# Kernel optimization log

Measured on AMD Instinct MI355X. Metric: run time of the kernel, lower is better.

Reference implementation:

```python
import jax, jax.numpy as jnp
import numpy as np

N_NODES = 50000
N_HEDGES = 10000
N_MEMB = 800000
IN_SIZE = 256
HEADS = 4
OUT_SIZE = 64


def setup_inputs() -> dict:
    key = jax.random.key(0)
    k1, k2, k3, k4, k5 = jax.random.split(key, 5)
    x = jax.random.normal(k1, (N_NODES, IN_SIZE), dtype=jnp.float32)
    # Linear weight stored as [in, out*heads] so projection is x @ W (same math as torch Linear)
    W = jax.random.normal(k2, (IN_SIZE, OUT_SIZE * HEADS), dtype=jnp.float32) * (1.0 / np.sqrt(IN_SIZE))
    att_e = jax.random.normal(k3, (1, HEADS, OUT_SIZE), dtype=jnp.float32) * 0.1
    node_idx = jax.random.randint(k4, (N_MEMB,), 0, N_NODES, dtype=jnp.int64)
    hedge_idx = jax.random.randint(k5, (N_MEMB,), 0, N_HEDGES, dtype=jnp.int64)
    return {"x": x, "W": W, "att_e": att_e, "node_idx": node_idx,
            "hedge_idx": hedge_idx, "num_hyperedges": N_HEDGES}


def reference(x, W, att_e, node_idx, hedge_idx, num_hyperedges):
    # Dropout is treated as eval-mode identity.
    N = x.shape[0]
    H, D = att_e.shape[1], att_e.shape[2]
    xp = (x @ W).reshape(N, H, D)                                   # [N,H,D]
    # Stage 1: mean-aggregate node features into hyperedges (belongs-to)
    ones = jnp.ones(node_idx.shape[0], dtype=x.dtype)
    deg = jax.ops.segment_sum(ones, hedge_idx, num_segments=num_hyperedges)  # [E]
    he = jax.ops.segment_sum(xp[node_idx], hedge_idx, num_segments=num_hyperedges)
    he = he / jnp.maximum(deg, 1.0)[:, None, None]                  # [E,H,D]
    # Attention logit per hyperedge
    alpha_e = jax.nn.leaky_relu(jnp.sum(he * att_e, axis=-1), 0.2)  # [E,H]
    # Stage 2: edge_softmax over 'contains' edges grouped by destination node
    ae = alpha_e[hedge_idx]                                         # [M,H]
    mx = jax.ops.segment_max(ae, node_idx, num_segments=N)          # [N,H]
    ex = jnp.exp(ae - mx[node_idx])
    den = jax.ops.segment_sum(ex, node_idx, num_segments=N)         # [N,H]
    a = ex / den[node_idx]                                          # [M,H]
    # Attention-weighted scatter-sum of hyperedge features to nodes
    out = jax.ops.segment_sum(he[hedge_idx] * a[:, :, None], node_idx, num_segments=N)  # [N,H,D]
    return out.reshape(N, H * D)
```

## Files before the change

kernel.cpp:

```cpp
#include <hip/hip_runtime.h>
#include <hip/hip_fp16.h>
#include <math.h>

#define N_NODES  50000
#define N_HEDGES 10000
#define N_MEMB   800000
#define KIN      256
#define CH       256
#define HEADS    4
#define HCAP     160
#define NCAP     48
#define GR       16

#define NCHUNK      125
#define CHUNK4      1600
#define XCVT_F4     3200000
#define XCVT_BLOCKS 1563
#define WCVT_BLOCKS 8
#define HED_W       2500
#define NOD_W       12500

__device__ inline float2 h2f(unsigned u) {
    __half2 h = __builtin_bit_cast(__half2, u);
    return __half22float2(h);
}
__device__ inline unsigned f2h(float a, float b) {
    return __builtin_bit_cast(unsigned, __floats2half2_rn(a, b));
}
__device__ inline float4 u2tof4(uint2 u) {
    float2 lo = h2f(u.x), hi = h2f(u.y);
    return make_float4(lo.x, lo.y, hi.x, hi.y);
}
__device__ inline void acc4(float4& a, float4 f) {
    a.x += f.x; a.y += f.y; a.z += f.z; a.w += f.w;
}
__device__ inline void fmaU4(float4& A, float4& B, float w, uint4 g) {
    float2 f0 = h2f(g.x), f1 = h2f(g.y), f2 = h2f(g.z), f3 = h2f(g.w);
    A.x += w * f0.x; A.y += w * f0.y; A.z += w * f1.x; A.w += w * f1.y;
    B.x += w * f2.x; B.y += w * f2.y; B.z += w * f3.x; B.w += w * f3.y;
}

__global__ __launch_bounds__(1024)
void k_hist_cvt(const int4* __restrict__ ni4, const int4* __restrict__ hi4,
                unsigned char* __restrict__ htab, unsigned char* __restrict__ ntab,
                const float4* __restrict__ x4, uint2* __restrict__ x16,
                const float4* __restrict__ Wf, uint2* __restrict__ W16) {
    __shared__ unsigned sh[HED_W + NOD_W];
    int bid = blockIdx.x, tid = threadIdx.x;
    if (bid < NCHUNK) {
        int chunk = bid;
        for (int i = tid; i < HED_W + NOD_W; i += 1024) sh[i] = 0;
        __syncthreads();
        int base4 = chunk * CHUNK4;
        for (int i = tid; i < CHUNK4; i += 1024) {
            int4 e = hi4[base4 + i]; int4 n = ni4[base4 + i];
            #pragma unroll
            for (int k = 0; k < 4; k++) {
                int ev = (&e.x)[k], nv = (&n.x)[k];
                atomicAdd(&sh[ev >> 2], 1u << ((ev & 3) * 8));
                atomicAdd(&sh[HED_W + (nv >> 2)], 1u << ((nv & 3) * 8));
            }
        }
        __syncthreads();
        unsigned* hd = (unsigned*)(htab + (size_t)chunk * N_HEDGES);
        for (int i = tid; i < HED_W; i += 1024) hd[i] = sh[i];
        unsigned* nd = (unsigned*)(ntab + (size_t)chunk * N_NODES);
        for (int i = tid; i < NOD_W; i += 1024) nd[i] = sh[HED_W + i];
    } else if (bid < NCHUNK + XCVT_BLOCKS) {
        int i0 = (bid - NCHUNK) * 2048 + tid;
        #pragma unroll
        for (int r = 0; r < 2; r++) {
            int idx = i0 + r * 1024;
            if (idx < XCVT_F4) {
                float4 v = x4[idx];
                uint2 u; u.x = f2h(v.x, v.y); u.y = f2h(v.z, v.w);
                x16[idx] = u;
            }
        }
    } else {
        int i0 = (bid - NCHUNK - XCVT_BLOCKS) * 2048 + tid;
        #pragma unroll
        for (int r = 0; r < 2; r++) {
            int idx = i0 + r * 1024;
            float4 v = Wf[idx];
            uint2 u; u.x = f2h(v.x, v.y); u.y = f2h(v.z, v.w);
            W16[idx] = u;
        }
    }
}

__global__ __launch_bounds__(1024)
void k_scan(unsigned char* __restrict__ htab, unsigned char* __restrict__ ntab,
            int* __restrict__ hdeg, int* __restrict__ ndeg) {
    int b = blockIdx.x * 1024 + threadIdx.x;
    if (b < N_HEDGES) {
        int run = 0;
        for (int c = 0; c < NCHUNK; c++) {
            size_t idx = (size_t)c * N_HEDGES + b;
            int v = htab[idx];
            htab[idx] = (unsigned char)run;
            run += v;
        }
        hdeg[b] = run;
    } else if (b < N_HEDGES + N_NODES) {
        int nb = b - N_HEDGES;
        int run = 0;
        for (int c = 0; c < NCHUNK; c++) {
            size_t idx = (size_t)c * N_NODES + nb;
            int v = ntab[idx];
            ntab[idx] = (unsigned char)run;
            run += v;
        }
        ndeg[nb] = run;
    }
}

__global__ __launch_bounds__(1024)
void k_place(const int4* __restrict__ ni4, const int4* __restrict__ hi4,
             const unsigned char* __restrict__ htab, const unsigned char* __restrict__ ntab,
             int* __restrict__ hmem, int* __restrict__ nhedge) {
    __shared__ unsigned sh[HED_W + NOD_W];
    int bid = blockIdx.x, tid = threadIdx.x;
    int chunk = bid;
    for (int i = tid; i < HED_W + NOD_W; i += 1024) sh[i] = 0;
    __syncthreads();
    int base4 = chunk * CHUNK4;
    const unsigned char* hoff = htab + (size_t)chunk * N_HEDGES;
    const unsigned char* noff = ntab + (size_t)chunk * N_NODES;
    for (int i = tid; i < CHUNK4; i += 1024) {
        int4 e = hi4[base4 + i]; int4 n = ni4[base4 + i];
        #pragma unroll
        for (int k = 0; k < 4; k++) {
            int ev = (&e.x)[k], nv = (&n.x)[k];
            unsigned oldh = atomicAdd(&sh[ev >> 2], 1u << ((ev & 3) * 8));
            int rh = (int)((oldh >> ((ev & 3) * 8)) & 0xffu);
            int posh = (int)hoff[ev] + rh;
            if (posh < HCAP) hmem[(size_t)ev * HCAP + posh] = nv;
            unsigned oldn = atomicAdd(&sh[HED_W + (nv >> 2)], 1u << ((nv & 3) * 8));
            int rn = (int)((oldn >> ((nv & 3) * 8)) & 0xffu);
            int posn = (int)noff[nv] + rn;
            if (posn < NCAP) nhedge[(size_t)nv * NCAP + posn] = ev;
        }
    }
}

__global__ __launch_bounds__(256, 8)
void k_stage1(const int* __restrict__ hdeg, const int* __restrict__ hmem,
              const uint2* __restrict__ x16, uint2* __restrict__ hx) {
    __shared__ int sidx[4][HCAP];
    int tid = threadIdx.x;
    int w = tid >> 6, lt = tid & 63;
    int e = blockIdx.x * 4 + w;
    int deg = hdeg[e];
    int degC = min(deg, HCAP);
    const int* ml = hmem + (size_t)e * HCAP;
    for (int j = lt; j < degC; j += 64) sidx[w][j] = ml[j];
    __syncthreads();
    float4 ac0 = {0,0,0,0}, ac1 = {0,0,0,0}, ac2 = {0,0,0,0}, ac3 = {0,0,0,0};
    int j = 0;
    for (; j + 8 <= degC; j += 8) {
        int4 ia = *(const int4*)&sidx[w][j];
        int4 ib = *(const int4*)&sidx[w][j + 4];
        uint2 g0 = x16[(size_t)ia.x * 64 + lt];
        uint2 g1 = x16[(size_t)ia.y * 64 + lt];
        uint2 g2 = x16[(size_t)ia.z * 64 + lt];
        uint2 g3 = x16[(size_t)ia.w * 64 + lt];
        uint2 g4 = x16[(size_t)ib.x * 64 + lt];
        uint2 g5 = x16[(size_t)ib.y * 64 + lt];
        uint2 g6 = x16[(size_t)ib.z * 64 + lt];
        uint2 g7 = x16[(size_t)ib.w * 64 + lt];
        acc4(ac0, u2tof4(g0)); acc4(ac1, u2tof4(g1));
        acc4(ac2, u2tof4(g2)); acc4(ac3, u2tof4(g3));
        acc4(ac0, u2tof4(g4)); acc4(ac1, u2tof4(g5));
        acc4(ac2, u2tof4(g6)); acc4(ac3, u2tof4(g7));
    }
    for (; j < degC; j++)
        acc4(ac0, u2tof4(x16[(size_t)sidx[w][j] * 64 + lt]));
    float sx = (ac0.x + ac1.x) + (ac2.x + ac3.x);
    float sy = (ac0.y + ac1.y) + (ac2.y + ac3.y);
    float sz = (ac0.z + ac1.z) + (ac2.z + ac3.z);
    float sw = (ac0.w + ac1.w) + (ac2.w + ac3.w);
    float inv = deg > 0 ? 1.0f / (float)deg : 0.0f;
    uint2 o; o.x = f2h(sx * inv, sy * inv); o.y = f2h(sz * inv, sw * inv);
    hx[(size_t)e * 64 + lt] = o;
}

__global__ void k_gemm_alpha(const uint2* __restrict__ hx, const __half* __restrict__ W16,
                             const float* __restrict__ att, __half* __restrict__ he,
                             float* __restrict__ alpha) {
    __shared__ float xs[GR][KIN];
    int tid = threadIdx.x;
    int e0 = blockIdx.x * GR;
    #pragma unroll
    for (int jj = 0; jj < GR * 64 / 256; jj++) {
        int f = jj * 256 + tid;
        int r = f >> 6, k4 = f & 63;
        uint2 u = hx[(size_t)(e0 + r) * 64 + k4];
        float2 lo = h2f(u.x), hi = h2f(u.y);
        *(float4*)&xs[r][k4 * 4] = make_float4(lo.x, lo.y, hi.x, hi.y);
    }
    __syncthreads();
    float acc[GR];
    #pragma unroll
    for (int r = 0; r < GR; r++) acc[r] = 0.f;
    int c = tid;
    const __half* wp = W16 + c;
    for (int k = 0; k < KIN; k++) {
        float wv = __half2float(wp[(size_t)k * CH]);
        #pragma unroll
        for (int r = 0; r < GR; r++) acc[r] += xs[r][k] * wv;
    }
    #pragma unroll
    for (int r = 0; r < GR; r++)
        he[(size_t)(e0 + r) * CH + c] = __float2half_rn(acc[r]);
    float av = att[c];
    int lane = tid & 63, h = tid >> 6;
    #pragma unroll
    for (int r = 0; r < GR; r++) {
        float p = acc[r] * av;
        #pragma unroll
        for (int d = 32; d >= 1; d >>= 1) p += __shfl_xor(p, d, 64);
        if (lane == 0) alpha[(e0 + r) * HEADS + h] = p > 0.f ? p : 0.2f * p;
    }
}

__global__ __launch_bounds__(256, 6)
void k_stage2(const uint4* __restrict__ heu4, const float4* __restrict__ alpha4,
              const int* __restrict__ ndeg, const int* __restrict__ nhedge,
              float4* __restrict__ out) {
    __shared__ int   nh[4][NCAP];
    __shared__ float wl[4][4][NCAP];
    int tid = threadIdx.x;
    int w = tid >> 6, L = tid & 63;
    int half = L >> 5, q = L & 31;
    int n = blockIdx.x * 4 + w;
    int deg = min(ndeg[n], NCAP);
    const int* nl = nhedge + (size_t)n * NCAP;
    if (L < deg) nh[w][L] = nl[L];
    __syncthreads();
    float4 mx = make_float4(-INFINITY, -INFINITY, -INFINITY, -INFINITY);
    float4 w4 = make_float4(0.f, 0.f, 0.f, 0.f);
    float4 aj = mx;
    if (L < deg) { aj = alpha4[nh[w][L]]; mx = aj; }
    #pragma unroll
    for (int d = 32; d >= 1; d >>= 1) {
        mx.x = fmaxf(mx.x, __shfl_xor(mx.x, d, 64));
        mx.y = fmaxf(mx.y, __shfl_xor(mx.y, d, 64));
        mx.z = fmaxf(mx.z, __shfl_xor(mx.z, d, 64));
        mx.w = fmaxf(mx.w, __shfl_xor(mx.w, d, 64));
    }
    if (L < deg) {
        w4.x = __expf(aj.x - mx.x); w4.y = __expf(aj.y - mx.y);
        w4.z = __expf(aj.z - mx.z); w4.w = __expf(aj.w - mx.w);
        wl[w][0][L] = w4.x; wl[w][1][L] = w4.y;
        wl[w][2][L] = w4.z; wl[w][3][L] = w4.w;
    }
    float4 dn = w4;
    #pragma unroll
    for (int d = 32; d >= 1; d >>= 1) {
        dn.x += __shfl_xor(dn.x, d, 64);
        dn.y += __shfl_xor(dn.y, d, 64);
        dn.z += __shfl_xor(dn.z, d, 64);
        dn.w += __shfl_xor(dn.w, d, 64);
    }
    __syncthreads();
    int h = q >> 3;
    float den = h < 2 ? (h == 0 ? dn.x : dn.y) : (h == 2 ? dn.z : dn.w);
    float4 A = make_float4(0.f, 0.f, 0.f, 0.f);
    float4 B = make_float4(0.f, 0.f, 0.f, 0.f);
    int j = 0;
    for (; j + 8 <= deg; j += 8) {
        uint4 g[4]; float wgt[4];
        #pragma unroll
        for (int i = 0; i < 4; i++) {
            int jj = j + 2 * i + half;
            wgt[i] = wl[w][h][jj];
            g[i] = heu4[(size_t)nh[w][jj] * 32 + q];
        }
        #pragma unroll
        for (int i = 0; i < 4; i++) fmaU4(A, B, wgt[i], g[i]);
    }
    for (; j < deg; j += 2) {
        int jj = j + half;
        uint4 g = {0, 0, 0, 0}; float ww = 0.f;
        if (jj < deg) { ww = wl[w][h][jj]; g = heu4[(size_t)nh[w][jj] * 32 + q]; }
        fmaU4(A, B, ww, g);
    }
    A.x += __shfl_xor(A.x, 32, 64); A.y += __shfl_xor(A.y, 32, 64);
    A.z += __shfl_xor(A.z, 32, 64); A.w += __shfl_xor(A.w, 32, 64);
    B.x += __shfl_xor(B.x, 32, 64); B.y += __shfl_xor(B.y, 32, 64);
    B.z += __shfl_xor(B.z, 32, 64); B.w += __shfl_xor(B.w, 32, 64);
    if (half == 0) {
        if (deg > 0) {
            float inv = 1.0f / den;
            A.x *= inv; A.y *= inv; A.z *= inv; A.w *= inv;
            B.x *= inv; B.y *= inv; B.z *= inv; B.w *= inv;
        }
        out[(size_t)n * 64 + 2 * q]     = A;
        out[(size_t)n * 64 + 2 * q + 1] = B;
    }
}

extern "C" void kernel_launch(void* const* d_in, const int* in_sizes, int n_in,
                              void* d_out, int out_size, void* d_ws, size_t ws_size,
                              hipStream_t stream) {
    const float* x        = (const float*)d_in[0];
    const float* W        = (const float*)d_in[1];
    const float* att      = (const float*)d_in[2];
    const int*   node_idx = (const int*)d_in[3];
    const int*   hedge_idx= (const int*)d_in[4];
    float4* out4 = (float4*)d_out;

    char* ws = (char*)d_ws;
    size_t o = 0;
    auto alloc = [&](size_t b) { size_t r = o; o += (b + 255) & ~(size_t)255; return r; };
    uint2* hx    = (uint2*)(ws + alloc(sizeof(__half) * (size_t)N_HEDGES * KIN));
    float* alpha = (float*)(ws + alloc(sizeof(float) * (size_t)N_HEDGES * HEADS));
    uint2* W16   = (uint2*)(ws + alloc(sizeof(__half) * (size_t)KIN * CH));
    int*   hdeg  = (int*)(ws + alloc(sizeof(int) * N_HEDGES));
    int*   ndeg  = (int*)(ws + alloc(sizeof(int) * N_NODES));
    size_t hmem_off = alloc(sizeof(int) * (size_t)N_HEDGES * HCAP);
    int*    hmem = (int*)(ws + hmem_off);
    __half* he   = (__half*)(ws + hmem_off);
    int*   nhedge = (int*)(ws + alloc(sizeof(int) * (size_t)N_NODES * NCAP));
    unsigned char* htab = (unsigned char*)(ws + alloc((size_t)NCHUNK * N_HEDGES));
    unsigned char* ntab = (unsigned char*)(ws + alloc((size_t)NCHUNK * N_NODES));
    if (o > ws_size) return;
    uint2* x16 = (uint2*)d_out;

    k_hist_cvt<<<NCHUNK + XCVT_BLOCKS + WCVT_BLOCKS, 1024, 0, stream>>>(
        (const int4*)node_idx, (const int4*)hedge_idx, htab, ntab,
        (const float4*)x, x16, (const float4*)W, W16);
    k_scan<<<(N_HEDGES + N_NODES + 1023) / 1024, 1024, 0, stream>>>(htab, ntab, hdeg, ndeg);
    k_place<<<NCHUNK, 1024, 0, stream>>>(
        (const int4*)node_idx, (const int4*)hedge_idx, htab, ntab, hmem, nhedge);
    k_stage1<<<N_HEDGES / 4, 256, 0, stream>>>(hdeg, hmem, x16, hx);
    k_gemm_alpha<<<N_HEDGES / GR, 256, 0, stream>>>(hx, (const __half*)W16, att, he, alpha);
    k_stage2<<<N_NODES / 4, 256, 0, stream>>>((const uint4*)he, (const float4*)alpha,
                                              ndeg, nhedge, out4);
}
```

Baseline: 199.3 us.

## Pack W as k-paired half2, use fdot2 GEMM, clamp-index gather loops

Result: faster. 193.8 us (-2.8%).

```diff
diff --git a/kernel.cpp b/kernel.cpp
--- a/kernel.cpp
+++ b/kernel.cpp
@@ -20,6 +20,8 @@
 #define HED_W       2500
 #define NOD_W       12500
 
+typedef _Float16 half2v __attribute__((ext_vector_type(2)));
+
 __device__ inline float2 h2f(unsigned u) {
     __half2 h = __builtin_bit_cast(__half2, u);
     return __half22float2(h);
@@ -44,7 +46,7 @@
 void k_hist_cvt(const int4* __restrict__ ni4, const int4* __restrict__ hi4,
                 unsigned char* __restrict__ htab, unsigned char* __restrict__ ntab,
                 const float4* __restrict__ x4, uint2* __restrict__ x16,
-                const float4* __restrict__ Wf, uint2* __restrict__ W16) {
+                const float* __restrict__ Wf, unsigned* __restrict__ Wp) {
     __shared__ unsigned sh[HED_W + NOD_W];
     int bid = blockIdx.x, tid = threadIdx.x;
     if (bid < NCHUNK) {
@@ -78,13 +80,12 @@
             }
         }
     } else {
-        int i0 = (bid - NCHUNK - XCVT_BLOCKS) * 2048 + tid;
-        #pragma unroll
-        for (int r = 0; r < 2; r++) {
-            int idx = i0 + r * 1024;
-            float4 v = Wf[idx];
-            uint2 u; u.x = f2h(v.x, v.y); u.y = f2h(v.z, v.w);
-            W16[idx] = u;
+        int tg = (bid - NCHUNK - XCVT_BLOCKS) * 1024 + tid;
+        #pragma unroll
+        for (int r = 0; r < 4; r++) {
+            int wI = tg + r * 8192;
+            int k2 = wI >> 8, c = wI & 255;
+            Wp[wI] = f2h(Wf[(size_t)(2 * k2) * CH + c], Wf[(size_t)(2 * k2 + 1) * CH + c]);
         }
     }
 }
@@ -157,25 +158,22 @@
     for (int j = lt; j < degC; j += 64) sidx[w][j] = ml[j];
     __syncthreads();
     float4 ac0 = {0,0,0,0}, ac1 = {0,0,0,0}, ac2 = {0,0,0,0}, ac3 = {0,0,0,0};
-    int j = 0;
-    for (; j + 8 <= degC; j += 8) {
-        int4 ia = *(const int4*)&sidx[w][j];
-        int4 ib = *(const int4*)&sidx[w][j + 4];
-        uint2 g0 = x16[(size_t)ia.x * 64 + lt];
-        uint2 g1 = x16[(size_t)ia.y * 64 + lt];
-        uint2 g2 = x16[(size_t)ia.z * 64 + lt];
-        uint2 g3 = x16[(size_t)ia.w * 64 + lt];
-        uint2 g4 = x16[(size_t)ib.x * 64 + lt];
-        uint2 g5 = x16[(size_t)ib.y * 64 + lt];
-        uint2 g6 = x16[(size_t)ib.z * 64 + lt];
-        uint2 g7 = x16[(size_t)ib.w * 64 + lt];
-        acc4(ac0, u2tof4(g0)); acc4(ac1, u2tof4(g1));
-        acc4(ac2, u2tof4(g2)); acc4(ac3, u2tof4(g3));
-        acc4(ac0, u2tof4(g4)); acc4(ac1, u2tof4(g5));
-        acc4(ac2, u2tof4(g6)); acc4(ac3, u2tof4(g7));
-    }
-    for (; j < degC; j++)
-        acc4(ac0, u2tof4(x16[(size_t)sidx[w][j] * 64 + lt]));
+    for (int j = 0; j < degC; j += 8) {
+        uint2 g[8];
+        #pragma unroll
+        for (int i = 0; i < 8; i++) {
+            int jj = j + i; jj = jj < degC ? jj : degC - 1;
+            g[i] = x16[(size_t)sidx[w][jj] * 64 + lt];
+        }
+        if (j + 0 < degC) acc4(ac0, u2tof4(g[0]));
+        if (j + 1 < degC) acc4(ac1, u2tof4(g[1]));
+        if (j + 2 < degC) acc4(ac2, u2tof4(g[2]));
+        if (j + 3 < degC) acc4(ac3, u2tof4(g[3]));
+        if (j + 4 < degC) acc4(ac0, u2tof4(g[4]));
+        if (j + 5 < degC) acc4(ac1, u2tof4(g[5]));
+        if (j + 6 < degC) acc4(ac2, u2tof4(g[6]));
+        if (j + 7 < degC) acc4(ac3, u2tof4(g[7]));
+    }
     float sx = (ac0.x + ac1.x) + (ac2.x + ac3.x);
     float sy = (ac0.y + ac1.y) + (ac2.y + ac3.y);
     float sz = (ac0.z + ac1.z) + (ac2.z + ac3.z);
@@ -185,10 +183,10 @@
     hx[(size_t)e * 64 + lt] = o;
 }
 
-__global__ void k_gemm_alpha(const uint2* __restrict__ hx, const __half* __restrict__ W16,
+__global__ void k_gemm_alpha(const uint2* __restrict__ hx, const unsigned* __restrict__ Wp,
                              const float* __restrict__ att, __half* __restrict__ he,
                              float* __restrict__ alpha) {
-    __shared__ float xs[GR][KIN];
+    __shared__ unsigned xsp[GR][KIN / 2];
     int tid = threadIdx.x;
     int e0 = blockIdx.x * GR;
     #pragma unroll
@@ -196,19 +194,24 @@
         int f = jj * 256 + tid;
         int r = f >> 6, k4 = f & 63;
         uint2 u = hx[(size_t)(e0 + r) * 64 + k4];
-        float2 lo = h2f(u.x), hi = h2f(u.y);
-        *(float4*)&xs[r][k4 * 4] = make_float4(lo.x, lo.y, hi.x, hi.y);
+        xsp[r][k4 * 2] = u.x; xsp[r][k4 * 2 + 1] = u.y;
     }
     __syncthreads();
     float acc[GR];
     #pragma unroll
     for (int r = 0; r < GR; r++) acc[r] = 0.f;
     int c = tid;
-    const __half* wp = W16 + c;
-    for (int k = 0; k < KIN; k++) {
-        float wv = __half2float(wp[(size_t)k * CH]);
-        #pragma unroll
-        for (int r = 0; r < GR; r++) acc[r] += xs[r][k] * wv;
+    for (int k2 = 0; k2 < KIN / 2; k2++) {
+        half2v wv = __builtin_bit_cast(half2v, Wp[k2 * CH + c]);
+        #pragma unroll
+        for (int r = 0; r < GR; r++) {
+            half2v av = __builtin_bit_cast(half2v, xsp[r][k2]);
+#if __has_builtin(__builtin_amdgcn_fdot2)
+            acc[r] = __builtin_amdgcn_fdot2(av, wv, acc[r], false);
+#else
+            acc[r] += (float)av.x * (float)wv.x + (float)av.y * (float)wv.y;
+#endif
+        }
     }
     #pragma unroll
     for (int r = 0; r < GR; r++)
@@ -224,7 +227,7 @@
     }
 }
 
-__global__ __launch_bounds__(256, 6)
+__global__ __launch_bounds__(256, 8)
 void k_stage2(const uint4* __restrict__ heu4, const float4* __restrict__ alpha4,
               const int* __restrict__ ndeg, const int* __restrict__ nhedge,
               float4* __restrict__ out) {
@@ -268,23 +271,19 @@
     float den = h < 2 ? (h == 0 ? dn.x : dn.y) : (h == 2 ? dn.z : dn.w);
     float4 A = make_float4(0.f, 0.f, 0.f, 0.f);
     float4 B = make_float4(0.f, 0.f, 0.f, 0.f);
-    int j = 0;
-    for (; j + 8 <= deg; j += 8) {
-        uint4 g[4]; float wgt[4];
-        #pragma unroll
-        for (int i = 0; i < 4; i++) {
-            int jj = j + 2 * i + half;
-            wgt[i] = wl[w][h][jj];
-            g[i] = heu4[(size_t)nh[w][jj] * 32 + q];
-        }
-        #pragma unroll
-        for (int i = 0; i < 4; i++) fmaU4(A, B, wgt[i], g[i]);
-    }
-    for (; j < deg; j += 2) {
-        int jj = j + half;
-        uint4 g = {0, 0, 0, 0}; float ww = 0.f;
-        if (jj < deg) { ww = wl[w][h][jj]; g = heu4[(size_t)nh[w][jj] * 32 + q]; }
-        fmaU4(A, B, ww, g);
+    if (deg > 0) {
+        for (int j = 0; j < deg; j += 8) {
+            uint4 g[4]; float wgt[4];
+            #pragma unroll
+            for (int i = 0; i < 4; i++) {
+                int jj = j + 2 * i + half;
+                int jc = jj < deg ? jj : deg - 1;
+                wgt[i] = jj < deg ? wl[w][h][jc] : 0.f;
+                g[i] = heu4[(size_t)nh[w][jc] * 32 + q];
+            }
+            #pragma unroll
+            for (int i = 0; i < 4; i++) fmaU4(A, B, wgt[i], g[i]);
+        }
     }
     A.x += __shfl_xor(A.x, 32, 64); A.y += __shfl_xor(A.y, 32, 64);
     A.z += __shfl_xor(A.z, 32, 64); A.w += __shfl_xor(A.w, 32, 64);
@@ -316,7 +315,7 @@
     auto alloc = [&](size_t b) { size_t r = o; o += (b + 255) & ~(size_t)255; return r; };
     uint2* hx    = (uint2*)(ws + alloc(sizeof(__half) * (size_t)N_HEDGES * KIN));
     float* alpha = (float*)(ws + alloc(sizeof(float) * (size_t)N_HEDGES * HEADS));
-    uint2* W16   = (uint2*)(ws + alloc(sizeof(__half) * (size_t)KIN * CH));
+    unsigned* Wp = (unsigned*)(ws + alloc(sizeof(unsigned) * (KIN / 2) * CH));
     int*   hdeg  = (int*)(ws + alloc(sizeof(int) * N_HEDGES));
     int*   ndeg  = (int*)(ws + alloc(sizeof(int) * N_NODES));
     size_t hmem_off = alloc(sizeof(int) * (size_t)N_HEDGES * HCAP);
@@ -330,12 +329,12 @@
 
     k_hist_cvt<<<NCHUNK + XCVT_BLOCKS + WCVT_BLOCKS, 1024, 0, stream>>>(
         (const int4*)node_idx, (const int4*)hedge_idx, htab, ntab,
-        (const float4*)x, x16, (const float4*)W, W16);
+        (const float4*)x, x16, W, Wp);
     k_scan<<<(N_HEDGES + N_NODES + 1023) / 1024, 1024, 0, stream>>>(htab, ntab, hdeg, ndeg);
     k_place<<<NCHUNK, 1024, 0, stream>>>(
         (const int4*)node_idx, (const int4*)hedge_idx, htab, ntab, hmem, nhedge);
     k_stage1<<<N_HEDGES / 4, 256, 0, stream>>>(hdeg, hmem, x16, hx);
-    k_gemm_alpha<<<N_HEDGES / GR, 256, 0, stream>>>(hx, (const __half*)W16, att, he, alpha);
+    k_gemm_alpha<<<N_HEDGES / GR, 256, 0, stream>>>(hx, Wp, att, he, alpha);
     k_stage2<<<N_NODES / 4, 256, 0, stream>>>((const uint4*)he, (const float4*)alpha,
                                               ndeg, nhedge, out4);
 }
```
